# Performance work log

Hardware: AMD Instinct MI355X
Metric: run time of the kernel (lower is better)

The kernel has to match this reference:

```python
import jax, jax.numpy as jnp
import numpy as np

SIZE = 32000
PAD_IDX = 0
SMOOTHING = 0.1
CONFIDENCE = 1.0 - SMOOTHING
NUM_EXPERTS = 8
LOAD_COEF = 0.01
Z_COEF = 0.001
NORMALIZE_LENGTH = True


def setup_inputs() -> dict:
    key = jax.random.key(0)
    k0, k1, k2, k3, k4 = jax.random.split(key, 5)
    B, S, K = 2, 2048, 2
    return {
        "x": jax.random.normal(k0, (B, S, SIZE), dtype=jnp.float32),
        "topk_values": jax.random.uniform(k1, (B, S, K), dtype=jnp.float32),
        "gate_logits": jax.random.normal(k2, (B, S, NUM_EXPERTS), dtype=jnp.float32),
        "target": jax.random.randint(k3, (B, S), 0, SIZE, dtype=jnp.int64),
        "topk_indices": jax.random.randint(k4, (B, S, K), 0, NUM_EXPERTS, dtype=jnp.int64),
    }


def reference(x, topk_values, gate_logits, target, topk_indices):
    # ---- label smoothing KLDiv ----
    xf = x.reshape(-1, SIZE)            # [N, V]
    t = target.reshape(-1)              # [N]
    N = xf.shape[0]
    ignore = t == PAD_IDX               # [N]
    total = N - ignore.sum()
    t0 = jnp.where(ignore, 0, t)
    smooth_val = SMOOTHING / (SIZE - 1)
    # true_dist built under torch.no_grad -> constant
    true_dist = jnp.full((N, SIZE), smooth_val, dtype=xf.dtype)
    true_dist = true_dist.at[jnp.arange(N), t0].set(CONFIDENCE)
    true_dist = jax.lax.stop_gradient(true_dist)
    logp = jax.nn.log_softmax(xf, axis=1)
    # KLDivLoss(reduction='none'): target * (log(target) - input)
    kl = true_dist * (jnp.log(true_dist) - logp)
    kl = jnp.where(ignore[:, None], jnp.zeros((), xf.dtype), kl)
    denom = total.astype(xf.dtype) if NORMALIZE_LENGTH else jnp.asarray(x.shape[0], xf.dtype)
    label_smoothing_loss = kl.sum() / denom

    # ---- load balancing loss (fused histogram instead of per-expert loop) ----
    # torch version uses .item() per expert -> fully detached from autodiff
    flat_idx = topk_indices.reshape(-1)
    expert_loads = jnp.zeros(NUM_EXPERTS, xf.dtype).at[flat_idx].add(1.0)
    logits_sum = jnp.zeros(NUM_EXPERTS, xf.dtype).at[flat_idx].add(topk_values.reshape(-1))
    num_elements = topk_indices.shape[0] * topk_indices.shape[1]
    load_loss = jax.lax.stop_gradient(
        (NUM_EXPERTS / num_elements) * (expert_loads * logits_sum).sum()
    )

    # ---- router z-loss ----
    router_z_loss = jnp.mean(jnp.square(jax.nn.logsumexp(gate_logits, axis=-1)))

    return label_smoothing_loss + LOAD_COEF * load_loss + Z_COEF * router_z_loss
```

## Files before the change

### kernel.cpp

```cpp
#include <hip/hip_runtime.h>
#include <hip/hip_bf16.h>
#include <math.h>

#define SIZE_V 32000
#define NROWS  4096
#define NEXP   8
#define NTOPK  8192
#define RBLK   320


__device__ inline float waveReduceSum(float v) {
#pragma unroll
    for (int off = 32; off; off >>= 1) v += __shfl_xor(v, off, 64);
    return v;
}

__global__ __launch_bounds__(RBLK) void row_kernel(const float* __restrict__ x,
                                                   const int* __restrict__ target,
                                                   const float* __restrict__ gate,
                                                   float* __restrict__ klrow,
                                                   float* __restrict__ zrow,
                                                   float self_ent, float smooth) {
    __shared__ float smS[5];
    __shared__ float smX[5];

    const int row = blockIdx.x;
    const int tid = threadIdx.x;
    const float4* xr = (const float4*)(x + (size_t)row * SIZE_V);

    int t = 0;
    float xt = 0.f;
    float4 ga = {0, 0, 0, 0}, gb = {0, 0, 0, 0};
    if (tid == 0) {
        t  = target[row];
        xt = x[(size_t)row * SIZE_V + t];
        const float4* gr = (const float4*)(gate + (size_t)row * NEXP);
        ga = gr[0];
        gb = gr[1];
    }

    float sAcc[5] = {0, 0, 0, 0, 0};
    float xAcc[5] = {0, 0, 0, 0, 0};
    float4 cur0, cur1, cur2, cur3, cur4;
    float4 nxt0, nxt1, nxt2, nxt3, nxt4;

    cur0 = xr[tid + 0 * RBLK];
    cur1 = xr[tid + 1 * RBLK];
    cur2 = xr[tid + 2 * RBLK];
    cur3 = xr[tid + 3 * RBLK];
    cur4 = xr[tid + 4 * RBLK];

    for (int j = 0; j < 5; ++j) {
        if (j < 4) {
            const int base = (j + 1) * 5;
            nxt0 = xr[tid + (base + 0) * RBLK];
            nxt1 = xr[tid + (base + 1) * RBLK];
            nxt2 = xr[tid + (base + 2) * RBLK];
            nxt3 = xr[tid + (base + 3) * RBLK];
            nxt4 = xr[tid + (base + 4) * RBLK];
        }
        sAcc[0] += (__expf(cur0.x) + __expf(cur0.y)) + (__expf(cur0.z) + __expf(cur0.w));
        xAcc[0] += (cur0.x + cur0.y) + (cur0.z + cur0.w);
        sAcc[1] += (__expf(cur1.x) + __expf(cur1.y)) + (__expf(cur1.z) + __expf(cur1.w));
        xAcc[1] += (cur1.x + cur1.y) + (cur1.z + cur1.w);
        sAcc[2] += (__expf(cur2.x) + __expf(cur2.y)) + (__expf(cur2.z) + __expf(cur2.w));
        xAcc[2] += (cur2.x + cur2.y) + (cur2.z + cur2.w);
        sAcc[3] += (__expf(cur3.x) + __expf(cur3.y)) + (__expf(cur3.z) + __expf(cur3.w));
        xAcc[3] += (cur3.x + cur3.y) + (cur3.z + cur3.w);
        sAcc[4] += (__expf(cur4.x) + __expf(cur4.y)) + (__expf(cur4.z) + __expf(cur4.w));
        xAcc[4] += (cur4.x + cur4.y) + (cur4.z + cur4.w);
        cur0 = nxt0; cur1 = nxt1; cur2 = nxt2; cur3 = nxt3; cur4 = nxt4;
    }
    float s  = ((sAcc[0] + sAcc[1]) + (sAcc[2] + sAcc[3])) + sAcc[4];
    float sx = ((xAcc[0] + xAcc[1]) + (xAcc[2] + xAcc[3])) + xAcc[4];

    const int lane = tid & 63, wid = tid >> 6;
    s  = waveReduceSum(s);
    sx = waveReduceSum(sx);
    if (lane == 0) { smS[wid] = s; smX[wid] = sx; }
    __syncthreads();

    if (tid == 0) {
        float S  = ((smS[0] + smS[1]) + (smS[2] + smS[3])) + smS[4];
        float SX = ((smX[0] + smX[1]) + (smX[2] + smX[3])) + smX[4];
        float logZ = __logf(S);
        float kl = 0.f;
        if (t != 0) {
            float sum_logp = SX - (float)SIZE_V * logZ;
            float logp_t = xt - logZ;
            kl = self_ent - (smooth * (sum_logp - logp_t) + 0.9f * logp_t);
        }
        klrow[row] = kl;

        float mx = fmaxf(fmaxf(fmaxf(ga.x, ga.y), fmaxf(ga.z, ga.w)),
                         fmaxf(fmaxf(gb.x, gb.y), fmaxf(gb.z, gb.w)));
        float se = __expf(ga.x - mx) + __expf(ga.y - mx) + __expf(ga.z - mx) + __expf(ga.w - mx)
                 + __expf(gb.x - mx) + __expf(gb.y - mx) + __expf(gb.z - mx) + __expf(gb.w - mx);
        float lse = mx + __logf(se);
        zrow[row] = lse * lse;
    }
}

__global__ __launch_bounds__(1024) void tail_kernel(const float* __restrict__ klrow,
                                                    const float* __restrict__ zrow,
                                                    const int* __restrict__ target,
                                                    const int* __restrict__ tidx,
                                                    const float* __restrict__ tval,
                                                    float* __restrict__ out) {
    __shared__ float sm[16][20];
    const int tid = threadIdx.x;

    float4 kv = ((const float4*)klrow)[tid];
    float4 zv = ((const float4*)zrow)[tid];
    int4   tv = ((const int4*)target)[tid];
    float kacc = (kv.x + kv.y) + (kv.z + kv.w);
    float zacc = (zv.x + zv.y) + (zv.z + zv.w);
    float cacc = ((tv.x != 0) ? 1.f : 0.f) + ((tv.y != 0) ? 1.f : 0.f)
               + ((tv.z != 0) ? 1.f : 0.f) + ((tv.w != 0) ? 1.f : 0.f);

    const int4*   ti4 = (const int4*)tidx;
    const float4* tv4 = (const float4*)tval;
    int4   e0 = ti4[tid * 2], e1 = ti4[tid * 2 + 1];
    float4 v0 = tv4[tid * 2], v1 = tv4[tid * 2 + 1];
    int   ee[8] = {e0.x, e0.y, e0.z, e0.w, e1.x, e1.y, e1.z, e1.w};
    float vv[8] = {v0.x, v0.y, v0.z, v0.w, v1.x, v1.y, v1.z, v1.w};

    float cnt[NEXP]  = {0, 0, 0, 0, 0, 0, 0, 0};
    float vsum[NEXP] = {0, 0, 0, 0, 0, 0, 0, 0};
#pragma unroll
    for (int i = 0; i < 8; i++) {
#pragma unroll
        for (int k = 0; k < NEXP; k++) {
            bool hit = (ee[i] == k);
            cnt[k]  += hit ? 1.f : 0.f;
            vsum[k] += hit ? vv[i] : 0.f;
        }
    }

    kacc = waveReduceSum(kacc);
    cacc = waveReduceSum(cacc);
    zacc = waveReduceSum(zacc);
#pragma unroll
    for (int k = 0; k < NEXP; k++) {
        cnt[k]  = waveReduceSum(cnt[k]);
        vsum[k] = waveReduceSum(vsum[k]);
    }

    const int lane = tid & 63, wid = tid >> 6;
    if (lane == 0) {
        sm[wid][0] = kacc;
        sm[wid][1] = cacc;
        sm[wid][2] = zacc;
#pragma unroll
        for (int k = 0; k < NEXP; k++) {
            sm[wid][3 + k]  = cnt[k];
            sm[wid][11 + k] = vsum[k];
        }
    }
    __syncthreads();

    if (tid == 0) {
        float KL = 0.f, TOT = 0.f, Z = 0.f;
        float C[NEXP] = {0, 0, 0, 0, 0, 0, 0, 0};
        float V[NEXP] = {0, 0, 0, 0, 0, 0, 0, 0};
        for (int w = 0; w < 16; w++) {
            KL += sm[w][0];
            TOT += sm[w][1];
            Z  += sm[w][2];
#pragma unroll
            for (int k = 0; k < NEXP; k++) {
                C[k] += sm[w][3 + k];
                V[k] += sm[w][11 + k];
            }
        }
        float dot = 0.f;
#pragma unroll
        for (int k = 0; k < NEXP; k++) dot += C[k] * V[k];

        float label = KL / TOT;
        float load  = ((float)NEXP / (float)NROWS) * dot;
        float z     = Z / (float)NROWS;
        out[0] = label + 0.01f * load + 0.001f * z;
    }
}

extern "C" void kernel_launch(void* const* d_in, const int* in_sizes, int n_in,
                              void* d_out, int out_size, void* d_ws, size_t ws_size,
                              hipStream_t stream) {
    const float* x      = (const float*)d_in[0];
    const float* tval   = (const float*)d_in[1];
    const float* gate   = (const float*)d_in[2];
    const int*   target = (const int*)d_in[3];
    const int*   tidx   = (const int*)d_in[4];
    float* out = (float*)d_out;
    float* klrow = (float*)d_ws;
    float* zrow  = (float*)d_ws + NROWS;

    const double sv = 0.1 / (double)(SIZE_V - 1);
    const float self_ent = (float)((double)(SIZE_V - 1) * sv * log(sv) + 0.9 * log(0.9));

    hipLaunchKernelGGL(row_kernel, dim3(NROWS), dim3(RBLK), 0, stream,
                       x, target, gate, klrow, zrow, self_ent, (float)sv);
    hipLaunchKernelGGL(tail_kernel, dim3(1), dim3(1024), 0, stream,
                       klrow, zrow, target, tidx, tval, out);
}
```

Before: 102.7 us.

## Split each row across five single-wave blocks and finalize KL in tail kernel

Each row reduction now runs as five independent 64-thread blocks, each covering one fifth of the vocabulary, instead of one 320-thread block. This removes the shared-memory exchange and block barrier. Partial exp-sums and x-sums go to workspace, and the tail kernel combines them and computes the per-row log-normalizer and KL term. The cost is more blocks, more partial traffic, and a heavier single-block tail kernel doing logs for every row.

```diff
diff --git a/kernel.cpp b/kernel.cpp
--- a/kernel.cpp
+++ b/kernel.cpp
@@ -6,7 +6,7 @@
 #define NROWS  4096
 #define NEXP   8
 #define NTOPK  8192
-#define RBLK   320
+#define NFIFTH 5
 
 
 __device__ inline float waveReduceSum(float v) {
@@ -15,23 +15,23 @@
     return v;
 }
 
-__global__ __launch_bounds__(RBLK) void row_kernel(const float* __restrict__ x,
-                                                   const int* __restrict__ target,
-                                                   const float* __restrict__ gate,
-                                                   float* __restrict__ klrow,
-                                                   float* __restrict__ zrow,
-                                                   float self_ent, float smooth) {
-    __shared__ float smS[5];
-    __shared__ float smX[5];
-
-    const int row = blockIdx.x;
+__global__ __launch_bounds__(64) void row_kernel(const float* __restrict__ x,
+                                                 const int* __restrict__ target,
+                                                 const float* __restrict__ gate,
+                                                 float* __restrict__ S5,
+                                                 float* __restrict__ SX5,
+                                                 float* __restrict__ XT,
+                                                 float* __restrict__ Z) {
+    const int b   = blockIdx.x;
+    const int row = b & (NROWS - 1);
+    const int f   = b >> 12;
     const int tid = threadIdx.x;
-    const float4* xr = (const float4*)(x + (size_t)row * SIZE_V);
+    const float4* xr = (const float4*)(x + (size_t)row * SIZE_V) + f * 1600;
 
     int t = 0;
     float xt = 0.f;
     float4 ga = {0, 0, 0, 0}, gb = {0, 0, 0, 0};
-    if (tid == 0) {
+    if (f == 0 && tid == 0) {
         t  = target[row];
         xt = x[(size_t)row * SIZE_V + t];
         const float4* gr = (const float4*)(gate + (size_t)row * NEXP);
@@ -44,20 +44,20 @@
     float4 cur0, cur1, cur2, cur3, cur4;
     float4 nxt0, nxt1, nxt2, nxt3, nxt4;
 
-    cur0 = xr[tid + 0 * RBLK];
-    cur1 = xr[tid + 1 * RBLK];
-    cur2 = xr[tid + 2 * RBLK];
-    cur3 = xr[tid + 3 * RBLK];
-    cur4 = xr[tid + 4 * RBLK];
+    cur0 = xr[tid + 0 * 64];
+    cur1 = xr[tid + 1 * 64];
+    cur2 = xr[tid + 2 * 64];
+    cur3 = xr[tid + 3 * 64];
+    cur4 = xr[tid + 4 * 64];
 
     for (int j = 0; j < 5; ++j) {
         if (j < 4) {
             const int base = (j + 1) * 5;
-            nxt0 = xr[tid + (base + 0) * RBLK];
-            nxt1 = xr[tid + (base + 1) * RBLK];
-            nxt2 = xr[tid + (base + 2) * RBLK];
-            nxt3 = xr[tid + (base + 3) * RBLK];
-            nxt4 = xr[tid + (base + 4) * RBLK];
+            nxt0 = xr[tid + (base + 0) * 64];
+            nxt1 = xr[tid + (base + 1) * 64];
+            nxt2 = xr[tid + (base + 2) * 64];
+            nxt3 = xr[tid + (base + 3) * 64];
+            nxt4 = xr[tid + (base + 4) * 64];
         }
         sAcc[0] += (__expf(cur0.x) + __expf(cur0.y)) + (__expf(cur0.z) + __expf(cur0.w));
         xAcc[0] += (cur0.x + cur0.y) + (cur0.z + cur0.w);
@@ -74,49 +74,65 @@
     float s  = ((sAcc[0] + sAcc[1]) + (sAcc[2] + sAcc[3])) + sAcc[4];
     float sx = ((xAcc[0] + xAcc[1]) + (xAcc[2] + xAcc[3])) + xAcc[4];
 
-    const int lane = tid & 63, wid = tid >> 6;
     s  = waveReduceSum(s);
     sx = waveReduceSum(sx);
-    if (lane == 0) { smS[wid] = s; smX[wid] = sx; }
-    __syncthreads();
 
     if (tid == 0) {
-        float S  = ((smS[0] + smS[1]) + (smS[2] + smS[3])) + smS[4];
-        float SX = ((smX[0] + smX[1]) + (smX[2] + smX[3])) + smX[4];
-        float logZ = __logf(S);
-        float kl = 0.f;
-        if (t != 0) {
-            float sum_logp = SX - (float)SIZE_V * logZ;
-            float logp_t = xt - logZ;
-            kl = self_ent - (smooth * (sum_logp - logp_t) + 0.9f * logp_t);
-        }
-        klrow[row] = kl;
-
-        float mx = fmaxf(fmaxf(fmaxf(ga.x, ga.y), fmaxf(ga.z, ga.w)),
-                         fmaxf(fmaxf(gb.x, gb.y), fmaxf(gb.z, gb.w)));
-        float se = __expf(ga.x - mx) + __expf(ga.y - mx) + __expf(ga.z - mx) + __expf(ga.w - mx)
-                 + __expf(gb.x - mx) + __expf(gb.y - mx) + __expf(gb.z - mx) + __expf(gb.w - mx);
-        float lse = mx + __logf(se);
-        zrow[row] = lse * lse;
-    }
-}
-
-__global__ __launch_bounds__(1024) void tail_kernel(const float* __restrict__ klrow,
-                                                    const float* __restrict__ zrow,
+        S5 [(f << 12) | row] = s;
+        SX5[(f << 12) | row] = sx;
+        if (f == 0) {
+            XT[row] = xt;
+            float mx = fmaxf(fmaxf(fmaxf(ga.x, ga.y), fmaxf(ga.z, ga.w)),
+                             fmaxf(fmaxf(gb.x, gb.y), fmaxf(gb.z, gb.w)));
+            float se = __expf(ga.x - mx) + __expf(ga.y - mx) + __expf(ga.z - mx) + __expf(ga.w - mx)
+                     + __expf(gb.x - mx) + __expf(gb.y - mx) + __expf(gb.z - mx) + __expf(gb.w - mx);
+            float lse = mx + __logf(se);
+            Z[row] = lse * lse;
+        }
+    }
+}
+
+__global__ __launch_bounds__(1024) void tail_kernel(const float* __restrict__ S5,
+                                                    const float* __restrict__ SX5,
+                                                    const float* __restrict__ XT,
+                                                    const float* __restrict__ Z,
                                                     const int* __restrict__ target,
                                                     const int* __restrict__ tidx,
                                                     const float* __restrict__ tval,
-                                                    float* __restrict__ out) {
+                                                    float* __restrict__ out,
+                                                    float self_ent, float smooth) {
     __shared__ float sm[16][20];
     const int tid = threadIdx.x;
 
-    float4 kv = ((const float4*)klrow)[tid];
-    float4 zv = ((const float4*)zrow)[tid];
-    int4   tv = ((const int4*)target)[tid];
-    float kacc = (kv.x + kv.y) + (kv.z + kv.w);
+    float4 Ssum = {0, 0, 0, 0}, Xsum = {0, 0, 0, 0};
+#pragma unroll
+    for (int f = 0; f < NFIFTH; f++) {
+        float4 sv = ((const float4*)(S5 + (f << 12)))[tid];
+        float4 xv = ((const float4*)(SX5 + (f << 12)))[tid];
+        Ssum.x += sv.x; Ssum.y += sv.y; Ssum.z += sv.z; Ssum.w += sv.w;
+        Xsum.x += xv.x; Xsum.y += xv.y; Xsum.z += xv.z; Xsum.w += xv.w;
+    }
+    float4 xtv = ((const float4*)XT)[tid];
+    float4 zv  = ((const float4*)Z)[tid];
+    int4   tv  = ((const int4*)target)[tid];
+
+    float Sr[4]  = {Ssum.x, Ssum.y, Ssum.z, Ssum.w};
+    float SXr[4] = {Xsum.x, Xsum.y, Xsum.z, Xsum.w};
+    float XTr[4] = {xtv.x, xtv.y, xtv.z, xtv.w};
+    int   Tr[4]  = {tv.x, tv.y, tv.z, tv.w};
+
+    float kacc = 0.f, cacc = 0.f;
     float zacc = (zv.x + zv.y) + (zv.z + zv.w);
-    float cacc = ((tv.x != 0) ? 1.f : 0.f) + ((tv.y != 0) ? 1.f : 0.f)
-               + ((tv.z != 0) ? 1.f : 0.f) + ((tv.w != 0) ? 1.f : 0.f);
+#pragma unroll
+    for (int c = 0; c < 4; c++) {
+        float logZ = __logf(Sr[c]);
+        if (Tr[c] != 0) {
+            float sum_logp = SXr[c] - (float)SIZE_V * logZ;
+            float logp_t = XTr[c] - logZ;
+            kacc += self_ent - (smooth * (sum_logp - logp_t) + 0.9f * logp_t);
+            cacc += 1.f;
+        }
+    }
 
     const int4*   ti4 = (const int4*)tidx;
     const float4* tv4 = (const float4*)tval;
@@ -160,13 +176,13 @@
     __syncthreads();
 
     if (tid == 0) {
-        float KL = 0.f, TOT = 0.f, Z = 0.f;
+        float KL = 0.f, TOT = 0.f, Zs = 0.f;
         float C[NEXP] = {0, 0, 0, 0, 0, 0, 0, 0};
         float V[NEXP] = {0, 0, 0, 0, 0, 0, 0, 0};
         for (int w = 0; w < 16; w++) {
             KL += sm[w][0];
             TOT += sm[w][1];
-            Z  += sm[w][2];
+            Zs += sm[w][2];
 #pragma unroll
             for (int k = 0; k < NEXP; k++) {
                 C[k] += sm[w][3 + k];
@@ -179,7 +195,7 @@
 
         float label = KL / TOT;
         float load  = ((float)NEXP / (float)NROWS) * dot;
-        float z     = Z / (float)NROWS;
+        float z     = Zs / (float)NROWS;
         out[0] = label + 0.01f * load + 0.001f * z;
     }
 }
@@ -193,14 +209,17 @@
     const int*   target = (const int*)d_in[3];
     const int*   tidx   = (const int*)d_in[4];
     float* out = (float*)d_out;
-    float* klrow = (float*)d_ws;
-    float* zrow  = (float*)d_ws + NROWS;
+    float* ws  = (float*)d_ws;
+    float* S5  = ws;
+    float* SX5 = ws + NFIFTH * NROWS;
+    float* XT  = ws + 2 * NFIFTH * NROWS;
+    float* Z   = XT + NROWS;
 
     const double sv = 0.1 / (double)(SIZE_V - 1);
     const float self_ent = (float)((double)(SIZE_V - 1) * sv * log(sv) + 0.9 * log(0.9));
 
-    hipLaunchKernelGGL(row_kernel, dim3(NROWS), dim3(RBLK), 0, stream,
-                       x, target, gate, klrow, zrow, self_ent, (float)sv);
+    hipLaunchKernelGGL(row_kernel, dim3(NFIFTH * NROWS), dim3(64), 0, stream,
+                       x, target, gate, S5, SX5, XT, Z);
     hipLaunchKernelGGL(tail_kernel, dim3(1), dim3(1024), 0, stream,
-                       klrow, zrow, target, tidx, tval, out);
-}
+                       S5, SX5, XT, Z, target, tidx, tval, out, self_ent, (float)sv);
+}
```

New measurement: 110.5 us. +7.6%, slower.
